# Performance work log

Measured on AMD Instinct MI355X. Metric: run time of the kernel, lower is better.

## Reference

```python
import jax, jax.numpy as jnp
import numpy as np

N = 100000       # nodes
E = 1600000      # edges (avg degree 16)
D = 128          # in_channels == hidden_channels (required for JK='sum')
L = 3            # num_layers
EPS = 1e-5       # BatchNorm eps


def setup_inputs() -> dict:
    key = jax.random.key(0)
    ks = jax.random.split(key, 6)
    x = jax.random.normal(ks[0], (N, D), dtype=jnp.float32)
    edge_index = jax.random.randint(ks[1], (2, E), 0, N, dtype=jnp.int32)
    W = jax.random.normal(ks[2], (L, D, D), dtype=jnp.float32) / np.sqrt(D)
    b = 0.01 * jax.random.normal(ks[3], (L, D), dtype=jnp.float32)
    gamma = 1.0 + 0.1 * jax.random.normal(ks[4], (L - 1, D), dtype=jnp.float32)
    beta = 0.1 * jax.random.normal(ks[5], (L - 1, D), dtype=jnp.float32)
    return {"x": x, "edge_index": edge_index, "W": W, "b": b,
            "gamma": gamma, "beta": beta}


def _gcn(h, src, dst, dinv, W_l, b_l):
    # PyG GCNConv: x@W, symmetric norm over A+I (self-loops), then +bias
    hw = h @ W_l                                   # [N, D]
    coef = (dinv[src] * dinv[dst])[:, None]        # [E, 1]
    agg = jax.ops.segment_sum(hw[src] * coef, dst, num_segments=N)
    agg = agg + hw * (dinv * dinv)[:, None]        # self-loop term
    return agg + b_l


def _bn_train(h, g, bt):
    # BatchNorm1d over nodes, training mode (batch stats, biased variance)
    m = jnp.mean(h, axis=0)
    v = jnp.mean((h - m) ** 2, axis=0)
    return (h - m) * jax.lax.rsqrt(v + EPS) * g + bt


def reference(x, edge_index, W, b, gamma, beta):
    src, dst = edge_index[0], edge_index[1]
    # degree of A+I based on destinations (PyG flow source_to_target)
    deg = jax.ops.segment_sum(jnp.ones((E,), x.dtype), dst, num_segments=N) + 1.0
    dinv = jax.lax.rsqrt(deg)
    h = x
    out = x                      # JK='sum' includes the input h_list[0]
    for l in range(L):
        h = jax.nn.relu(_gcn(h, src, dst, dinv, W[l], b[l]))
        # dropout p=0.0 -> identity
        if l != L - 1:
            h = _bn_train(h, gamma[l], beta[l])
        out = out + h
    return out
```

## Files before the change

kernel.cpp:

```cpp
#include <hip/hip_runtime.h>
#include <hip/hip_bf16.h>


constexpr int NN = 100000;
constexpr int EE = 1600000;
constexpr int DD = 128;
constexpr float BN_EPS = 1e-5f;
constexpr int NPAD = 100096;
constexpr int SPMM_GRID = NN / 16;
constexpr int GEMM_GRID = (NN + 63) / 64;
constexpr int BNRED_GRID = 250;

constexpr int NBK = (NN + 511) / 512;
constexpr int PB = 4096;
constexpr int PART_GRID = (EE + PB - 1) / PB;
constexpr int CSTRIDE = 400;
constexpr int CAPL = 10240;

typedef __attribute__((ext_vector_type(8))) short bf16x8;
typedef __attribute__((ext_vector_type(4))) float f32x4;

__device__ __forceinline__ float bfhi(unsigned int u) {
  union { unsigned int i; float f; } v; v.i = u & 0xffff0000u; return v.f;
}
__device__ __forceinline__ float bflo(unsigned int u) {
  union { unsigned int i; float f; } v; v.i = u << 16; return v.f;
}
__device__ __forceinline__ unsigned short f2bf(float f) {
  union { float f; unsigned int i; } v;
  v.f = f;
  unsigned int r = v.i + 0x7FFFu + ((v.i >> 16) & 1u);
  return (unsigned short)(r >> 16);
}
__device__ __forceinline__ unsigned pack2(float lo, float hi) {
  return (unsigned)f2bf(lo) | ((unsigned)f2bf(hi) << 16);
}
__device__ __forceinline__ void accu8(uint2 u, float sc, float4& a0, float4& a1) {
  a0.x = fmaf(sc, (float)(u.x & 0xffu), a0.x);
  a0.y = fmaf(sc, (float)((u.x >> 8) & 0xffu), a0.y);
  a0.z = fmaf(sc, (float)((u.x >> 16) & 0xffu), a0.z);
  a0.w = fmaf(sc, (float)(u.x >> 24), a0.w);
  a1.x = fmaf(sc, (float)(u.y & 0xffu), a1.x);
  a1.y = fmaf(sc, (float)((u.y >> 8) & 0xffu), a1.y);
  a1.z = fmaf(sc, (float)((u.y >> 16) & 0xffu), a1.z);
  a1.w = fmaf(sc, (float)(u.y >> 24), a1.w);
}
__device__ __forceinline__ int wave_incl_scan(int v, int lane) {
#pragma unroll
  for (int off = 1; off < 64; off <<= 1) {
    int x = __shfl_up(v, off, 64);
    if (lane >= off) v += x;
  }
  return v;
}

__global__ __launch_bounds__(256)
void k_cnt(const int* __restrict__ dst, int* __restrict__ cntT) {
  __shared__ int cnt[256];
  const int t = threadIdx.x;
  const int e0 = blockIdx.x * PB;
  const int nv = min(PB, EE - e0);
  cnt[t] = 0;
  __syncthreads();
  for (int i = t; i < nv; i += 256)
    atomicAdd(&cnt[dst[e0 + i] >> 9], 1);
  __syncthreads();
  if (t < NBK) cntT[t * CSTRIDE + blockIdx.x] = cnt[t];
}

__global__ __launch_bounds__(64)
void k_colscan(const int* __restrict__ cntT, int* __restrict__ baseT,
               int* __restrict__ gtot) {
  const int b = blockIdx.x;
  const int lane = threadIdx.x;
  int c[7];
  int ls = 0;
#pragma unroll
  for (int j = 0; j < 7; ++j) {
    const int idx = lane * 7 + j;
    c[j] = (idx < PART_GRID) ? cntT[b * CSTRIDE + idx] : 0;
    ls += c[j];
  }
  const int is = wave_incl_scan(ls, lane);
  int run = is - ls;
#pragma unroll
  for (int j = 0; j < 7; ++j) {
    const int idx = lane * 7 + j;
    if (idx < PART_GRID) baseT[b * CSTRIDE + idx] = run;
    run += c[j];
  }
  if (lane == 63) gtot[b] = is;
}

__global__ __launch_bounds__(256)
void k_part2(const int* __restrict__ src, const int* __restrict__ dst,
             const int* __restrict__ baseT, const int* __restrict__ gtot,
             unsigned* __restrict__ ebuf) {
  __shared__ unsigned sorted[PB];
  __shared__ unsigned char sortedb[PB];
  alignas(16) __shared__ int cnt[256];
  __shared__ int cur[256], start[256], gbase[256];
  __shared__ int bktb[200];
  const int t = threadIdx.x;
  const int lane = t & 63;
  const int e0 = blockIdx.x * PB;
  const int nv = min(PB, EE - e0);
  cnt[t] = 0;
  if (t < 64) {
    int c[4];
    int ls = 0;
#pragma unroll
    for (int j = 0; j < 4; ++j) {
      const int idx = t * 4 + j;
      c[j] = (idx < NBK) ? gtot[idx] : 0;
      ls += c[j];
    }
    const int is = wave_incl_scan(ls, t);
    int run = is - ls;
#pragma unroll
    for (int j = 0; j < 4; ++j) {
      const int idx = t * 4 + j;
      if (idx < NBK) bktb[idx] = run;
      run += c[j];
    }
  }
  __syncthreads();
  if (t < NBK) gbase[t] = bktb[t] + baseT[t * CSTRIDE + blockIdx.x];
  int es[PB / 256], ed[PB / 256];
#pragma unroll
  for (int j = 0; j < PB / 256; ++j) {
    const int i = t + j * 256;
    if (i < nv) {
      es[j] = src[e0 + i];
      ed[j] = dst[e0 + i];
      atomicAdd(&cnt[ed[j] >> 9], 1);
    } else {
      ed[j] = -1;
    }
  }
  __syncthreads();
  if (t < 64) {
    const int4 c = *(const int4*)&cnt[lane * 4];
    const int ls = c.x + c.y + c.z + c.w;
    const int is = wave_incl_scan(ls, lane);
    int run = is - ls;
    start[lane * 4] = run; cur[lane * 4] = run; run += c.x;
    start[lane * 4 + 1] = run; cur[lane * 4 + 1] = run; run += c.y;
    start[lane * 4 + 2] = run; cur[lane * 4 + 2] = run; run += c.z;
    start[lane * 4 + 3] = run; cur[lane * 4 + 3] = run;
  }
  __syncthreads();
#pragma unroll
  for (int j = 0; j < PB / 256; ++j) {
    if (ed[j] >= 0) {
      const int bkt = ed[j] >> 9;
      const int p = atomicAdd(&cur[bkt], 1);
      sorted[p] = ((unsigned)es[j] << 9) | (unsigned)(ed[j] & 511);
      sortedb[p] = (unsigned char)bkt;
    }
  }
  __syncthreads();
  for (int i = t; i < nv; i += 256) {
    const int bkt = sortedb[i];
    ebuf[(size_t)gbase[bkt] + (i - start[bkt])] = sorted[i];
  }
}

__global__ __launch_bounds__(256)
void k_csr2(const unsigned* __restrict__ ebuf, const int* __restrict__ gtot,
            int* __restrict__ rowptr, int* __restrict__ col,
            float* __restrict__ dinv) {
  __shared__ int rowcnt[512], rowbase[512], rowcur[512];
  __shared__ int bktb[200];
  __shared__ unsigned colseg[CAPL];
  const int b = blockIdx.x;
  const int t = threadIdx.x;
  if (t < 64) {
    int c[4];
    int ls = 0;
#pragma unroll
    for (int j = 0; j < 4; ++j) {
      const int idx = t * 4 + j;
      c[j] = (idx < NBK) ? gtot[idx] : 0;
      ls += c[j];
    }
    const int is = wave_incl_scan(ls, t);
    int run = is - ls;
#pragma unroll
    for (int j = 0; j < 4; ++j) {
      const int idx = t * 4 + j;
      if (idx < NBK) bktb[idx] = run;
      run += c[j];
    }
    if (t == 63) bktb[NBK] = is;
  }
  rowcnt[t] = 0;
  rowcnt[t + 256] = 0;
  __syncthreads();
  const int ebase = bktb[b];
  const int n = min(bktb[b + 1] - ebase, CAPL);
  const unsigned* eb = &ebuf[ebase];
  for (int i = t; i < n; i += 256)
    atomicAdd(&rowcnt[eb[i] & 511u], 1);
  __syncthreads();
  if (t < 64) {
    int v[8];
    int ls = 0;
#pragma unroll
    for (int j = 0; j < 8; ++j) { v[j] = rowcnt[t * 8 + j]; ls += v[j]; }
    const int is = wave_incl_scan(ls, t);
    int run = is - ls;
#pragma unroll
    for (int j = 0; j < 8; ++j) {
      rowbase[t * 8 + j] = run;
      rowcur[t * 8 + j] = run;
      run += v[j];
    }
  }
  __syncthreads();
#pragma unroll
  for (int h = 0; h < 2; ++h) {
    const int rl = t + h * 256;
    const int r = b * 512 + rl;
    if (r < NN) {
      rowptr[r] = ebase + rowbase[rl];
      dinv[r] = rsqrtf((float)rowcnt[rl] + 1.0f);
    }
  }
  if (b == NBK - 1 && t == 0) rowptr[NN] = ebase + n;
  for (int i = t; i < n; i += 256) {
    const unsigned u = eb[i];
    const int p = atomicAdd(&rowcur[u & 511u], 1);
    colseg[p] = u >> 9;
  }
  __syncthreads();
  for (int i = t; i < n; i += 256) col[ebase + i] = (int)colseg[i];
}

__global__ __launch_bounds__(256)
void k_wt(const float* __restrict__ W, unsigned short* __restrict__ Wt) {
  const float* Ws = W + (size_t)blockIdx.x * DD * DD;
  unsigned short* Wo = Wt + (size_t)blockIdx.x * DD * DD;
  for (int i = threadIdx.x; i < DD * DD; i += 256) {
    const int k = i >> 7, c = i & 127;
    Wo[c * DD + k] = f2bf(Ws[i]);
  }
}

__global__ __launch_bounds__(256)
void k_gemm(const float* __restrict__ hf, const unsigned short* __restrict__ hb,
            const unsigned short* __restrict__ Wt,
            const float* __restrict__ dinv, unsigned char* __restrict__ hs8,
            float* __restrict__ scalev, const float* __restrict__ ss) {
  const int lane = threadIdx.x & 63;
  const int wave = threadIdx.x >> 6;
  const int n15 = lane & 15;
  const int quad = lane >> 4;
  const int rbase = blockIdx.x * 64 + wave * 16;
  const int r0 = rbase + n15;
  const int arow = (r0 < NN) ? r0 : NN - 1;

  f32x4 acc[8];
#pragma unroll
  for (int ct = 0; ct < 8; ++ct) acc[ct] = (f32x4){0.f, 0.f, 0.f, 0.f};

#pragma unroll
  for (int kc = 0; kc < 4; ++kc) {
    const int k0 = kc * 32 + quad * 8;
    float4 a0, a1;
    if (hb) {
      const uint4 u = *(const uint4*)&hb[(size_t)arow * DD + k0];
      a0.x = bflo(u.x); a0.y = bfhi(u.x);
      a0.z = bflo(u.y); a0.w = bfhi(u.y);
      a1.x = bflo(u.z); a1.y = bfhi(u.z);
      a1.z = bflo(u.w); a1.w = bfhi(u.w);
    } else {
      a0 = *(const float4*)&hf[(size_t)arow * DD + k0];
      a1 = *(const float4*)&hf[(size_t)arow * DD + k0 + 4];
    }
    if (ss) {
      const float4 sc0 = *(const float4*)&ss[k0];
      const float4 sc1 = *(const float4*)&ss[k0 + 4];
      const float4 sh0 = *(const float4*)&ss[128 + k0];
      const float4 sh1 = *(const float4*)&ss[128 + k0 + 4];
      a0.x = fmaf(a0.x, sc0.x, sh0.x); a0.y = fmaf(a0.y, sc0.y, sh0.y);
      a0.z = fmaf(a0.z, sc0.z, sh0.z); a0.w = fmaf(a0.w, sc0.w, sh0.w);
      a1.x = fmaf(a1.x, sc1.x, sh1.x); a1.y = fmaf(a1.y, sc1.y, sh1.y);
      a1.z = fmaf(a1.z, sc1.z, sh1.z); a1.w = fmaf(a1.w, sc1.w, sh1.w);
    }
    bf16x8 af;
    af[0] = (short)f2bf(a0.x); af[1] = (short)f2bf(a0.y);
    af[2] = (short)f2bf(a0.z); af[3] = (short)f2bf(a0.w);
    af[4] = (short)f2bf(a1.x); af[5] = (short)f2bf(a1.y);
    af[6] = (short)f2bf(a1.z); af[7] = (short)f2bf(a1.w);
#pragma unroll
    for (int ct = 0; ct < 8; ++ct) {
      const bf16x8 bf = *(const bf16x8*)&Wt[(size_t)(ct * 16 + n15) * DD + k0];
      acc[ct] = __builtin_amdgcn_mfma_f32_16x16x32_bf16(af, bf, acc[ct], 0, 0, 0);
    }
  }

#pragma unroll
  for (int i = 0; i < 4; ++i) {
    const int r = rbase + quad * 4 + i;
    const int rr = (r < NN) ? r : NN - 1;
    const float dv = dinv[rr];
    float v[8];
    float m = 0.f;
#pragma unroll
    for (int ct = 0; ct < 8; ++ct) {
      v[ct] = acc[ct][i] * dv;
      m = fmaxf(m, fabsf(v[ct]));
    }
#pragma unroll
    for (int off = 1; off < 16; off <<= 1)
      m = fmaxf(m, __shfl_xor(m, off, 64));
    const float inv = (m > 0.f) ? 127.0f / m : 0.f;
    if (r < NN) {
#pragma unroll
      for (int ct = 0; ct < 8; ++ct) {
        const int q = __float2int_rn(v[ct] * inv) + 128;
        hs8[(size_t)r * DD + ct * 16 + n15] = (unsigned char)(q & 0xff);
      }
      if (n15 == 0) scalev[r] = m * (1.0f / 127.0f);
    }
  }
}

__global__ __launch_bounds__(256)
void k_spmm(const unsigned char* __restrict__ hs8,
            const float* __restrict__ scalev, const int* __restrict__ rowptr,
            const int* __restrict__ col, const float* __restrict__ dinv,
            const float* __restrict__ bias, unsigned short* __restrict__ hout,
            float* __restrict__ partials, const float* __restrict__ x,
            const unsigned short* __restrict__ h1b,
            const unsigned short* __restrict__ h2b,
            const float* __restrict__ ss, float* __restrict__ out,
            const int mode) {
  const int lane = threadIdx.x & 15;
  const int g = threadIdx.x >> 4;
  const int c8 = lane * 8;
  const int d = blockIdx.x * 16 + g;
  float4 a0 = make_float4(0.f, 0.f, 0.f, 0.f);
  float4 a1 = make_float4(0.f, 0.f, 0.f, 0.f);
  float4 c0 = a0, c1 = a0;
  float ssA = 0.f, ssB = 0.f;
  float4 bs0 = a0, bs1 = a0, q0 = a0, q1 = a0;
  if (d < NN) {
    {
      const float sc = scalev[d];
      accu8(*(const uint2*)&hs8[(size_t)d * DD + c8], sc, a0, a1);
      ssA += sc;
    }
    int j = rowptr[d];
    const int e1 = rowptr[d + 1];
    for (; j + 7 < e1; j += 8) {
      const int s0 = col[j],     s1 = col[j + 1], s2 = col[j + 2], s3 = col[j + 3];
      const int s4 = col[j + 4], s5 = col[j + 5], s6 = col[j + 6], s7 = col[j + 7];
      const uint2 u0 = *(const uint2*)&hs8[(size_t)s0 * DD + c8];
      const uint2 u1 = *(const uint2*)&hs8[(size_t)s1 * DD + c8];
      const uint2 u2 = *(const uint2*)&hs8[(size_t)s2 * DD + c8];
      const uint2 u3 = *(const uint2*)&hs8[(size_t)s3 * DD + c8];
      const uint2 u4 = *(const uint2*)&hs8[(size_t)s4 * DD + c8];
      const uint2 u5 = *(const uint2*)&hs8[(size_t)s5 * DD + c8];
      const uint2 u6 = *(const uint2*)&hs8[(size_t)s6 * DD + c8];
      const uint2 u7 = *(const uint2*)&hs8[(size_t)s7 * DD + c8];
      const float f0 = scalev[s0], f1 = scalev[s1], f2 = scalev[s2], f3 = scalev[s3];
      const float f4 = scalev[s4], f5 = scalev[s5], f6 = scalev[s6], f7 = scalev[s7];
      accu8(u0, f0, a0, a1); ssA += f0;
      accu8(u1, f1, c0, c1); ssB += f1;
      accu8(u2, f2, a0, a1); ssA += f2;
      accu8(u3, f3, c0, c1); ssB += f3;
      accu8(u4, f4, a0, a1); ssA += f4;
      accu8(u5, f5, c0, c1); ssB += f5;
      accu8(u6, f6, a0, a1); ssA += f6;
      accu8(u7, f7, c0, c1); ssB += f7;
    }
    for (; j + 3 < e1; j += 4) {
      const int s0 = col[j], s1 = col[j + 1], s2 = col[j + 2], s3 = col[j + 3];
      const uint2 u0 = *(const uint2*)&hs8[(size_t)s0 * DD + c8];
      const uint2 u1 = *(const uint2*)&hs8[(size_t)s1 * DD + c8];
      const uint2 u2 = *(const uint2*)&hs8[(size_t)s2 * DD + c8];
      const uint2 u3 = *(const uint2*)&hs8[(size_t)s3 * DD + c8];
      const float f0 = scalev[s0], f1 = scalev[s1], f2 = scalev[s2], f3 = scalev[s3];
      accu8(u0, f0, a0, a1); ssA += f0;
      accu8(u1, f1, c0, c1); ssB += f1;
      accu8(u2, f2, a0, a1); ssA += f2;
      accu8(u3, f3, c0, c1); ssB += f3;
    }
    for (; j < e1; ++j) {
      const int s0 = col[j];
      const float f0 = scalev[s0];
      accu8(*(const uint2*)&hs8[(size_t)s0 * DD + c8], f0, a0, a1);
      ssA += f0;
    }
    a0.x += c0.x; a0.y += c0.y; a0.z += c0.z; a0.w += c0.w;
    a1.x += c1.x; a1.y += c1.y; a1.z += c1.z; a1.w += c1.w;
    const float corr = 128.0f * (ssA + ssB);
    a0.x -= corr; a0.y -= corr; a0.z -= corr; a0.w -= corr;
    a1.x -= corr; a1.y -= corr; a1.z -= corr; a1.w -= corr;
    const float dv = dinv[d];
    const float4 bb0 = *(const float4*)&bias[c8];
    const float4 bb1 = *(const float4*)&bias[c8 + 4];
    float4 o0, o1;
    o0.x = fmaxf(fmaf(a0.x, dv, bb0.x), 0.f);
    o0.y = fmaxf(fmaf(a0.y, dv, bb0.y), 0.f);
    o0.z = fmaxf(fmaf(a0.z, dv, bb0.z), 0.f);
    o0.w = fmaxf(fmaf(a0.w, dv, bb0.w), 0.f);
    o1.x = fmaxf(fmaf(a1.x, dv, bb1.x), 0.f);
    o1.y = fmaxf(fmaf(a1.y, dv, bb1.y), 0.f);
    o1.z = fmaxf(fmaf(a1.z, dv, bb1.z), 0.f);
    o1.w = fmaxf(fmaf(a1.w, dv, bb1.w), 0.f);
    if (mode == 0) {
      uint4 pk;
      pk.x = pack2(o0.x, o0.y); pk.y = pack2(o0.z, o0.w);
      pk.z = pack2(o1.x, o1.y); pk.w = pack2(o1.z, o1.w);
      *(uint4*)&hout[(size_t)d * DD + c8] = pk;
      bs0 = o0; bs1 = o1;
      q0.x = o0.x * o0.x; q0.y = o0.y * o0.y;
      q0.z = o0.z * o0.z; q0.w = o0.w * o0.w;
      q1.x = o1.x * o1.x; q1.y = o1.y * o1.y;
      q1.z = o1.z * o1.z; q1.w = o1.w * o1.w;
    } else {
      float4 v0 = *(const float4*)&x[(size_t)d * DD + c8];
      float4 v1 = *(const float4*)&x[(size_t)d * DD + c8 + 4];
      const uint4 uh1 = *(const uint4*)&h1b[(size_t)d * DD + c8];
      const uint4 uh2 = *(const uint4*)&h2b[(size_t)d * DD + c8];
      {
        const float4 sc0 = *(const float4*)&ss[c8];
        const float4 sc1 = *(const float4*)&ss[c8 + 4];
        const float4 sh0 = *(const float4*)&ss[128 + c8];
        const float4 sh1 = *(const float4*)&ss[128 + c8 + 4];
        v0.x += fmaf(bflo(uh1.x), sc0.x, sh0.x);
        v0.y += fmaf(bfhi(uh1.x), sc0.y, sh0.y);
        v0.z += fmaf(bflo(uh1.y), sc0.z, sh0.z);
        v0.w += fmaf(bfhi(uh1.y), sc0.w, sh0.w);
        v1.x += fmaf(bflo(uh1.z), sc1.x, sh1.x);
        v1.y += fmaf(bfhi(uh1.z), sc1.y, sh1.y);
        v1.z += fmaf(bflo(uh1.w), sc1.z, sh1.z);
        v1.w += fmaf(bfhi(uh1.w), sc1.w, sh1.w);
      }
      {
        const float4 sc0 = *(const float4*)&ss[256 + c8];
        const float4 sc1 = *(const float4*)&ss[256 + c8 + 4];
        const float4 sh0 = *(const float4*)&ss[384 + c8];
        const float4 sh1 = *(const float4*)&ss[384 + c8 + 4];
        v0.x += fmaf(bflo(uh2.x), sc0.x, sh0.x);
        v0.y += fmaf(bfhi(uh2.x), sc0.y, sh0.y);
        v0.z += fmaf(bflo(uh2.y), sc0.z, sh0.z);
        v0.w += fmaf(bfhi(uh2.y), sc0.w, sh0.w);
        v1.x += fmaf(bflo(uh2.z), sc1.x, sh1.x);
        v1.y += fmaf(bfhi(uh2.z), sc1.y, sh1.y);
        v1.z += fmaf(bflo(uh2.w), sc1.z, sh1.z);
        v1.w += fmaf(bfhi(uh2.w), sc1.w, sh1.w);
      }
      v0.x += o0.x; v0.y += o0.y; v0.z += o0.z; v0.w += o0.w;
      v1.x += o1.x; v1.y += o1.y; v1.z += o1.z; v1.w += o1.w;
      *(float4*)&out[(size_t)d * DD + c8] = v0;
      *(float4*)&out[(size_t)d * DD + c8 + 4] = v1;
    }
  }
  if (mode == 0) {
    __shared__ float red[256 * 16];
    float* my = &red[threadIdx.x * 16];
    my[0] = bs0.x; my[1] = bs0.y; my[2] = bs0.z; my[3] = bs0.w;
    my[4] = bs1.x; my[5] = bs1.y; my[6] = bs1.z; my[7] = bs1.w;
    my[8] = q0.x;  my[9] = q0.y;  my[10] = q0.z; my[11] = q0.w;
    my[12] = q1.x; my[13] = q1.y; my[14] = q1.z; my[15] = q1.w;
    __syncthreads();
    const int t = threadIdx.x;
    float s = 0.f;
#pragma unroll
    for (int gg = 0; gg < 16; ++gg) s += red[gg * 256 + t];
    partials[(size_t)blockIdx.x * 256 + t] = s;
  }
}

__global__ __launch_bounds__(256)
void k_bnred(const float* __restrict__ partials, float* __restrict__ stat2) {
  const int t = threadIdx.x;
  const int j = blockIdx.x;
  float v = 0.f;
#pragma unroll 5
  for (int r = 0; r < 25; ++r)
    v += partials[(size_t)(j * 25 + r) * 256 + t];
  stat2[(size_t)j * 256 + t] = v;
}

__global__ __launch_bounds__(256)
void k_bnfin(const float* __restrict__ stat2, float* __restrict__ ss,
             const float* __restrict__ gamma, const float* __restrict__ beta) {
  __shared__ float tot[256];
  const int t = threadIdx.x;
  float s = 0.f;
  for (int j = 0; j < BNRED_GRID; ++j)
    s += stat2[(size_t)j * 256 + t];
  const int lane16 = t >> 4, q = t & 15;
  const int c = lane16 * 8 + (q & 7), kind = q >> 3;
  tot[kind * 128 + c] = s;
  __syncthreads();
  if (t < 128) {
    const float m = tot[t] * (1.0f / NN);
    const float var = tot[128 + t] * (1.0f / NN) - m * m;
    const float rs = rsqrtf(var + BN_EPS);
    const float sc = rs * gamma[t];
    ss[t] = sc;
    ss[128 + t] = beta[t] - m * sc;
  }
}

extern "C" void kernel_launch(void* const* d_in, const int* in_sizes, int n_in,
                              void* d_out, int out_size, void* d_ws, size_t ws_size,
                              hipStream_t stream) {
  const float* x = (const float*)d_in[0];
  const int* ei = (const int*)d_in[1];
  const float* W = (const float*)d_in[2];
  const float* b = (const float*)d_in[3];
  const float* gamma = (const float*)d_in[4];
  const float* beta = (const float*)d_in[5];
  float* out = (float*)d_out;
  const int* srcv = ei;
  const int* dstv = ei + EE;

  char* w = (char*)d_ws;
  int* rowptr = (int*)w;     w += (size_t)NPAD * 4;
  float* dinv = (float*)w;   w += (size_t)NPAD * 4;
  float* scalev = (float*)w; w += (size_t)NPAD * 4;
  int* cntT = (int*)w;       w += (size_t)NBK * CSTRIDE * 4;
  int* baseT = (int*)w;      w += (size_t)NBK * CSTRIDE * 4;
  int* gtot = (int*)w;       w += 256 * 4;
  float* ss = (float*)w;     w += 512 * 4;
  float* stat2 = (float*)w;  w += (size_t)BNRED_GRID * 256 * 4;
  int* col = (int*)w;        w += (size_t)EE * 4;
  unsigned short* Wt = (unsigned short*)w; w += (size_t)3 * DD * DD * 2;
  unsigned* ebuf = (unsigned*)w;
  float* partials = (float*)w; w += (size_t)EE * 4;
  unsigned short* h1b = (unsigned short*)w; w += (size_t)NN * DD * 2;
  unsigned short* h2b = (unsigned short*)w; w += (size_t)NN * DD * 2;
  unsigned char* hs8 = (unsigned char*)w;

  k_cnt<<<PART_GRID, 256, 0, stream>>>(dstv, cntT);
  k_colscan<<<NBK, 64, 0, stream>>>(cntT, baseT, gtot);
  k_part2<<<PART_GRID, 256, 0, stream>>>(srcv, dstv, baseT, gtot, ebuf);
  k_csr2<<<NBK, 256, 0, stream>>>(ebuf, gtot, rowptr, col, dinv);
  k_wt<<<3, 256, 0, stream>>>(W, Wt);

  k_gemm<<<GEMM_GRID, 256, 0, stream>>>(x, nullptr, Wt, dinv, hs8, scalev,
                                        nullptr);
  k_spmm<<<SPMM_GRID, 256, 0, stream>>>(hs8, scalev, rowptr, col, dinv, b,
                                        h1b, partials,
                                        nullptr, nullptr, nullptr, nullptr,
                                        nullptr, 0);
  k_bnred<<<BNRED_GRID, 256, 0, stream>>>(partials, stat2);
  k_bnfin<<<1, 256, 0, stream>>>(stat2, ss, gamma, beta);

  k_gemm<<<GEMM_GRID, 256, 0, stream>>>(nullptr, h1b, Wt + (size_t)DD * DD,
                                        dinv, hs8, scalev, ss);
  k_spmm<<<SPMM_GRID, 256, 0, stream>>>(hs8, scalev, rowptr, col, dinv, b + DD,
                                        h2b, partials,
                                        nullptr, nullptr, nullptr, nullptr,
                                        nullptr, 0);
  k_bnred<<<BNRED_GRID, 256, 0, stream>>>(partials, stat2);
  k_bnfin<<<1, 256, 0, stream>>>(stat2, ss + 256, gamma + DD, beta + DD);

  k_gemm<<<GEMM_GRID, 256, 0, stream>>>(nullptr, h2b, Wt + (size_t)2 * DD * DD,
                                        dinv, hs8, scalev, ss + 256);
  k_spmm<<<SPMM_GRID, 256, 0, stream>>>(hs8, scalev, rowptr, col, dinv,
                                        b + 2 * DD, nullptr, nullptr,
                                        x, h1b, h2b, ss, out, 1);
}
```

Before: 449.0 us.

## Sort destination rows by degree for balanced SpMM row scheduling

Builds a per-block degree histogram during CSR construction, scans it, and scatters rows into a degree-sorted permutation. The SpMM kernels then process rows through that permutation, so each 16-row block holds rows of similar degree, which is meant to cut wave divergence and tail imbalance. In exchange it adds two small kernels, an indirection load per row, and a loss of output and neighbour locality, since rows in a block are no longer contiguous. That extra scattering of writes to hout and partials could hurt.

New measurement: 471.1 us. 1.05x slower.

```diff
diff --git a/kernel.cpp b/kernel.cpp
--- a/kernel.cpp
+++ b/kernel.cpp
@@ -16,6 +16,8 @@
 constexpr int PART_GRID = (EE + PB - 1) / PB;
 constexpr int CSTRIDE = 400;
 constexpr int CAPL = 10240;
+constexpr int DSTRIDE = 200;
+constexpr int DBINS = 64;
 
 typedef __attribute__((ext_vector_type(8))) short bf16x8;
 typedef __attribute__((ext_vector_type(4))) float f32x4;
@@ -169,9 +171,10 @@
 __global__ __launch_bounds__(256)
 void k_csr2(const unsigned* __restrict__ ebuf, const int* __restrict__ gtot,
             int* __restrict__ rowptr, int* __restrict__ col,
-            float* __restrict__ dinv) {
+            float* __restrict__ dinv, int* __restrict__ cntD) {
   __shared__ int rowcnt[512], rowbase[512], rowcur[512];
   __shared__ int bktb[200];
+  __shared__ int dh[DBINS];
   __shared__ unsigned colseg[CAPL];
   const int b = blockIdx.x;
   const int t = threadIdx.x;
@@ -196,6 +199,7 @@
   }
   rowcnt[t] = 0;
   rowcnt[t + 256] = 0;
+  if (t < DBINS) dh[t] = 0;
   __syncthreads();
   const int ebase = bktb[b];
   const int n = min(bktb[b + 1] - ebase, CAPL);
@@ -225,6 +229,7 @@
     if (r < NN) {
       rowptr[r] = ebase + rowbase[rl];
       dinv[r] = rsqrtf((float)rowcnt[rl] + 1.0f);
+      atomicAdd(&dh[min(rowcnt[rl], DBINS - 1)], 1);
     }
   }
   if (b == NBK - 1 && t == 0) rowptr[NN] = ebase + n;
@@ -235,6 +240,55 @@
   }
   __syncthreads();
   for (int i = t; i < n; i += 256) col[ebase + i] = (int)colseg[i];
+  if (t < DBINS) cntD[t * DSTRIDE + b] = dh[t];
+}
+
+__global__ __launch_bounds__(256)
+void k_dscan(const int* __restrict__ cntD, int* __restrict__ baseD) {
+  __shared__ int csum[256];
+  const int t = threadIdx.x;
+  constexpr int TOT = DBINS * NBK;
+  constexpr int PERT = (TOT + 255) / 256;
+  int s = 0;
+  for (int i = 0; i < PERT; ++i) {
+    const int idx = t * PERT + i;
+    if (idx < TOT) s += cntD[(idx / NBK) * DSTRIDE + (idx % NBK)];
+  }
+  csum[t] = s;
+  __syncthreads();
+  if (t == 0) {
+    int run = 0;
+    for (int i = 0; i < 256; ++i) { const int v = csum[i]; csum[i] = run; run += v; }
+  }
+  __syncthreads();
+  int run = csum[t];
+  for (int i = 0; i < PERT; ++i) {
+    const int idx = t * PERT + i;
+    if (idx < TOT) {
+      const int d = idx / NBK, bb = idx % NBK;
+      baseD[d * DSTRIDE + bb] = run;
+      run += cntD[d * DSTRIDE + bb];
+    }
+  }
+}
+
+__global__ __launch_bounds__(256)
+void k_dscat(const int* __restrict__ rowptr, const int* __restrict__ baseD,
+             int* __restrict__ rowperm) {
+  __shared__ int cur[DBINS];
+  const int b = blockIdx.x;
+  const int t = threadIdx.x;
+  if (t < DBINS) cur[t] = baseD[t * DSTRIDE + b];
+  __syncthreads();
+#pragma unroll
+  for (int h = 0; h < 2; ++h) {
+    const int r = b * 512 + t + h * 256;
+    if (r < NN) {
+      const int deg = min(rowptr[r + 1] - rowptr[r], DBINS - 1);
+      const int p = atomicAdd(&cur[deg], 1);
+      rowperm[p] = r;
+    }
+  }
 }
 
 __global__ __launch_bounds__(256)
@@ -331,6 +385,7 @@
 void k_spmm(const unsigned char* __restrict__ hs8,
             const float* __restrict__ scalev, const int* __restrict__ rowptr,
             const int* __restrict__ col, const float* __restrict__ dinv,
+            const int* __restrict__ rowperm,
             const float* __restrict__ bias, unsigned short* __restrict__ hout,
             float* __restrict__ partials, const float* __restrict__ x,
             const unsigned short* __restrict__ h1b,
@@ -340,13 +395,13 @@
   const int lane = threadIdx.x & 15;
   const int g = threadIdx.x >> 4;
   const int c8 = lane * 8;
-  const int d = blockIdx.x * 16 + g;
+  const int d = rowperm[blockIdx.x * 16 + g];
   float4 a0 = make_float4(0.f, 0.f, 0.f, 0.f);
   float4 a1 = make_float4(0.f, 0.f, 0.f, 0.f);
   float4 c0 = a0, c1 = a0;
   float ssA = 0.f, ssB = 0.f;
   float4 bs0 = a0, bs1 = a0, q0 = a0, q1 = a0;
-  if (d < NN) {
+  {
     {
       const float sc = scalev[d];
       accu8(*(const uint2*)&hs8[(size_t)d * DD + c8], sc, a0, a1);
@@ -526,8 +581,11 @@
   int* rowptr = (int*)w;     w += (size_t)NPAD * 4;
   float* dinv = (float*)w;   w += (size_t)NPAD * 4;
   float* scalev = (float*)w; w += (size_t)NPAD * 4;
+  int* rowperm = (int*)w;    w += (size_t)NPAD * 4;
   int* cntT = (int*)w;       w += (size_t)NBK * CSTRIDE * 4;
   int* baseT = (int*)w;      w += (size_t)NBK * CSTRIDE * 4;
+  int* cntD = (int*)w;       w += (size_t)DBINS * DSTRIDE * 4;
+  int* baseD = (int*)w;      w += (size_t)DBINS * DSTRIDE * 4;
   int* gtot = (int*)w;       w += 256 * 4;
   float* ss = (float*)w;     w += 512 * 4;
   float* stat2 = (float*)w;  w += (size_t)BNRED_GRID * 256 * 4;
@@ -542,13 +600,15 @@
   k_cnt<<<PART_GRID, 256, 0, stream>>>(dstv, cntT);
   k_colscan<<<NBK, 64, 0, stream>>>(cntT, baseT, gtot);
   k_part2<<<PART_GRID, 256, 0, stream>>>(srcv, dstv, baseT, gtot, ebuf);
-  k_csr2<<<NBK, 256, 0, stream>>>(ebuf, gtot, rowptr, col, dinv);
+  k_csr2<<<NBK, 256, 0, stream>>>(ebuf, gtot, rowptr, col, dinv, cntD);
+  k_dscan<<<1, 256, 0, stream>>>(cntD, baseD);
+  k_dscat<<<NBK, 256, 0, stream>>>(rowptr, baseD, rowperm);
   k_wt<<<3, 256, 0, stream>>>(W, Wt);
 
   k_gemm<<<GEMM_GRID, 256, 0, stream>>>(x, nullptr, Wt, dinv, hs8, scalev,
                                         nullptr);
-  k_spmm<<<SPMM_GRID, 256, 0, stream>>>(hs8, scalev, rowptr, col, dinv, b,
-                                        h1b, partials,
+  k_spmm<<<SPMM_GRID, 256, 0, stream>>>(hs8, scalev, rowptr, col, dinv,
+                                        rowperm, b, h1b, partials,
                                         nullptr, nullptr, nullptr, nullptr,
                                         nullptr, 0);
   k_bnred<<<BNRED_GRID, 256, 0, stream>>>(partials, stat2);
@@ -556,8 +616,8 @@
 
   k_gemm<<<GEMM_GRID, 256, 0, stream>>>(nullptr, h1b, Wt + (size_t)DD * DD,
                                         dinv, hs8, scalev, ss);
-  k_spmm<<<SPMM_GRID, 256, 0, stream>>>(hs8, scalev, rowptr, col, dinv, b + DD,
-                                        h2b, partials,
+  k_spmm<<<SPMM_GRID, 256, 0, stream>>>(hs8, scalev, rowptr, col, dinv,
+                                        rowperm, b + DD, h2b, partials,
                                         nullptr, nullptr, nullptr, nullptr,
                                         nullptr, 0);
   k_bnred<<<BNRED_GRID, 256, 0, stream>>>(partials, stat2);
@@ -566,6 +626,6 @@
   k_gemm<<<GEMM_GRID, 256, 0, stream>>>(nullptr, h2b, Wt + (size_t)2 * DD * DD,
                                         dinv, hs8, scalev, ss + 256);
   k_spmm<<<SPMM_GRID, 256, 0, stream>>>(hs8, scalev, rowptr, col, dinv,
-                                        b + 2 * DD, nullptr, nullptr,
+                                        rowperm, b + 2 * DD, nullptr, nullptr,
                                         x, h1b, h2b, ss, out, 1);
 }
```
